# Kernel optimization log

Measured on AMD Instinct MI355X. Metric: run time of the kernel, lower is better.

Reference implementation:

```python
import jax, jax.numpy as jnp
import numpy as np

B, H, S, DK = 4, 16, 4096, 64


def setup_inputs() -> dict:
    key = jax.random.key(0)
    kq, kk, kv = jax.random.split(key, 3)
    Q = jax.random.normal(kq, (B, H, S, DK), dtype=jnp.float32)
    K = jax.random.normal(kk, (B, H, S, DK), dtype=jnp.float32)
    V = jax.random.normal(kv, (B, H, S, DK), dtype=jnp.float32)
    return {"Q": Q, "K": K, "V": V}


def reference(Q, K, V):
    d_k = K.shape[-1]
    inv_sqrt_dk = jnp.sqrt(jnp.float32(1.0) / d_k)
    # [B, H, S, S] materialized scores (faithful to the naive original)
    scores = jnp.einsum('bhqd,bhkd->bhqk', Q, K) * inv_sqrt_dk
    # causal mask: original subtracts (1 - tril) * 1e9 from scores
    s_q, s_k = Q.shape[-2], K.shape[-2]
    causal = jnp.tril(jnp.ones((s_q, s_k), dtype=jnp.float32))
    scores = scores - (1.0 - causal) * 1e9
    probs = jax.nn.softmax(scores, axis=-1)
    out = jnp.einsum('bhqk,bhkd->bhqd', probs, V)
    return out
```

## Files before the change

### kernel.cpp

```cpp
#include <hip/hip_runtime.h>
#include <hip/hip_bf16.h>

typedef short bf16x8 __attribute__((ext_vector_type(8)));
typedef float f32x16 __attribute__((ext_vector_type(16)));
typedef float f32x4v __attribute__((ext_vector_type(4)));

static constexpr int SEQ = 4096;
static constexpr int HD  = 64;
static constexpr int BQ  = 128;
static constexpr int BK  = 64;
static constexpr float QSCALE = 0.125f * 1.44269504088896340736f;

union F8 { bf16x8 v; unsigned short u[8]; uint4 q; };

__device__ __forceinline__ unsigned short f2bf(float x) {
    __bf16 b = (__bf16)x;
    return __builtin_bit_cast(unsigned short, b);
}
__device__ __forceinline__ unsigned pk2(float lo, float hi) {
    return (unsigned)f2bf(lo) | ((unsigned)f2bf(hi) << 16);
}
__device__ __forceinline__ float exp2fast(float x) {
    return __builtin_amdgcn_exp2f(x);
}

__global__ __launch_bounds__(256)
void prep_kv(const float* __restrict__ K, const float* __restrict__ V,
             unsigned short* __restrict__ ws)
{
    __shared__ float vt[64][68];

    const int tid = threadIdx.x;
    const int bid = blockIdx.x;
    const size_t sbase = ((size_t)(bid >> 6)) * (SEQ * HD) +
                         ((size_t)(bid & 63)) * (64 * HD);
    unsigned short* Kt = ws + (size_t)bid * 4096;
    unsigned short* Vt = ws + (size_t)16777216 + (size_t)bid * 4096;

    #pragma unroll
    for (int i = 0; i < 2; ++i) {
        const int c   = tid + 256 * i;
        const int row = c >> 3, j = c & 7;
        const int jsrc = j ^ (row & 7);
        const float* src = K + sbase + row * HD + 8 * jsrc;
        float4 a = *(const float4*)src;
        float4 b = *(const float4*)(src + 4);
        *(uint4*)(Kt + row * 64 + 8 * j) =
            make_uint4(pk2(a.x, a.y), pk2(a.z, a.w), pk2(b.x, b.y), pk2(b.z, b.w));
    }

    {
        const int r  = tid >> 2;
        const int cb = (tid & 3) << 4;
        const float* src = V + sbase + r * HD + cb;
        *(float4*)&vt[r][cb + 0]  = *(const float4*)(src);
        *(float4*)&vt[r][cb + 4]  = *(const float4*)(src + 4);
        *(float4*)&vt[r][cb + 8]  = *(const float4*)(src + 8);
        *(float4*)&vt[r][cb + 12] = *(const float4*)(src + 12);
    }
    __syncthreads();
    #pragma unroll
    for (int i = 0; i < 2; ++i) {
        const int c = tid + 256 * i;
        const int d = c >> 3, j = c & 7;
        const int kb = 8 * (j ^ (d & 7));
        unsigned u[4];
        #pragma unroll
        for (int p = 0; p < 4; ++p)
            u[p] = pk2(vt[kb + 2 * p][d], vt[kb + 2 * p + 1][d]);
        *(uint4*)(Vt + d * 64 + 8 * j) = make_uint4(u[0], u[1], u[2], u[3]);
    }
}

template<bool PRE>
__global__ __launch_bounds__(256, 4)
void mha_fwd(const float* __restrict__ Q, const float* __restrict__ K,
             const float* __restrict__ V, float* __restrict__ O,
             const unsigned short* __restrict__ ws)
{
    __shared__ unsigned short Kl[2][4096];
    __shared__ unsigned short Vl[2][4096];

    const int tid  = threadIdx.x;
    const int lane = tid & 63;
    const int w    = tid >> 6;
    const int l31  = lane & 31;
    const int h    = lane >> 5;

    const int bid = blockIdx.x;
    const int bh  = bid & 63;
    const int qb  = 31 - (bid >> 6);
    const int q0  = qb * BQ;
    const size_t base = (size_t)bh * (SEQ * HD);

    const int qlane  = q0 + 32 * w + l31;
    const int qmax_w = q0 + 32 * w + 31;

    bf16x8 qf[4];
    {
        const float* qrow = Q + base + (size_t)qlane * HD;
        #pragma unroll
        for (int c = 0; c < 4; ++c) {
            const f32x4v x = *(const f32x4v*)(qrow + 16 * c + 8 * h);
            const f32x4v y = *(const f32x4v*)(qrow + 16 * c + 8 * h + 4);
            F8 f;
            #pragma unroll
            for (int j = 0; j < 4; ++j) f.u[j]     = f2bf(x[j] * QSCALE);
            #pragma unroll
            for (int j = 0; j < 4; ++j) f.u[4 + j] = f2bf(y[j] * QSCALE);
            qf[c] = f.v;
        }
    }

    F8 onesf;
    #pragma unroll
    for (int j = 0; j < 8; ++j) onesf.u[j] = 0x3F80;

    f32x16 oacc[2];
    f32x16 lacc;
    #pragma unroll
    for (int r = 0; r < 16; ++r) { oacc[0][r] = 0.f; oacc[1][r] = 0.f; lacc[r] = 0.f; }

    const int nkt = 2 * qb + 2;

    const int ksr = tid >> 2;
    const int ksc = (tid & 3) << 4;
    const int vkb = tid >> 4;
    const int vdb = tid & 15;

    f32x4v kreg[4], vreg[4];

    const unsigned short* Kws = ws;
    const unsigned short* Vws = ws + (size_t)16777216;

    auto stage_pre = [&](int buf, int kt) {
        const size_t toff = (((size_t)bh << 6) + (size_t)kt) << 12;
        #pragma unroll
        for (int i = 0; i < 2; ++i) {
            const int ch = 2 * w + i;
            const unsigned short* kg = Kws + toff + ch * 512 + lane * 8;
            const unsigned short* vg = Vws + toff + ch * 512 + lane * 8;
            __builtin_amdgcn_global_load_lds(
                (const __attribute__((address_space(1))) void*)(const void*)kg,
                (__attribute__((address_space(3))) void*)(void*)&Kl[buf][ch * 512],
                16, 0, 0);
            __builtin_amdgcn_global_load_lds(
                (const __attribute__((address_space(1))) void*)(const void*)vg,
                (__attribute__((address_space(3))) void*)(void*)&Vl[buf][ch * 512],
                16, 0, 0);
        }
    };

    auto load_regs = [&](int kt) {
        const int k0 = kt * BK;
        const float* ks = K + base + (size_t)(k0 + ksr) * HD + ksc;
        kreg[0] = *(const f32x4v*)(ks);
        kreg[1] = *(const f32x4v*)(ks + 4);
        kreg[2] = *(const f32x4v*)(ks + 8);
        kreg[3] = *(const f32x4v*)(ks + 12);
        const float* vs = V + base + (size_t)(k0 + 4 * vkb) * HD + 4 * vdb;
        vreg[0] = *(const f32x4v*)(vs);
        vreg[1] = *(const f32x4v*)(vs + HD);
        vreg[2] = *(const f32x4v*)(vs + 2 * HD);
        vreg[3] = *(const f32x4v*)(vs + 3 * HD);
    };

    auto write_lds = [&](int buf) {
        unsigned u[8];
        #pragma unroll
        for (int i = 0; i < 4; ++i) {
            u[2*i]   = pk2(kreg[i][0], kreg[i][1]);
            u[2*i+1] = pk2(kreg[i][2], kreg[i][3]);
        }
        char* kd = (char*)&Kl[buf][0] + ksr * 128;
        const int o0 = (2 * ksc) ^ ((ksr & 7) << 4);
        *(uint4*)(kd + o0)        = make_uint4(u[0], u[1], u[2], u[3]);
        *(uint4*)(kd + (o0 ^ 16)) = make_uint4(u[4], u[5], u[6], u[7]);
        #pragma unroll
        for (int i = 0; i < 4; ++i) {
            const int c = (i + (vdb >> 1)) & 3;
            const int d = 4 * vdb + c;
            const unsigned lo = pk2(vreg[0][c], vreg[1][c]);
            const unsigned hi = pk2(vreg[2][c], vreg[3][c]);
            char* vd = (char*)&Vl[buf][0] + d * 128 + ((8 * vkb) ^ ((d & 7) << 4));
            *(uint2*)vd = make_uint2(lo, hi);
        }
    };

    if constexpr (PRE) { stage_pre(0, 0); }
    else               { load_regs(0); write_lds(0); }
    __syncthreads();

    for (int kt = 0; kt < nkt; ++kt) {
        const int cur = kt & 1;
        const bool hn = (kt + 1) < nkt;
        if constexpr (PRE) { if (hn) stage_pre(cur ^ 1, kt + 1); }
        else               { if (hn) load_regs(kt + 1); }

        if (64 * kt <= qmax_w) {
            const unsigned short* Kb = &Kl[cur][0];
            const unsigned short* Vb = &Vl[cur][0];
            const int k0 = kt * BK;

            f32x16 sacc[2];
            #pragma unroll
            for (int s = 0; s < 2; ++s)
                #pragma unroll
                for (int r = 0; r < 16; ++r) sacc[s][r] = 0.f;

            #pragma unroll
            for (int s = 0; s < 2; ++s) {
                const int row = 32 * s + l31;
                const char* rp = (const char*)Kb + row * 128;
                const int sw = (row & 7) << 4;
                #pragma unroll
                for (int c = 0; c < 4; ++c) {
                    bf16x8 kf = *(const bf16x8*)(rp + ((32 * c + 16 * h) ^ sw));
                    sacc[s] = __builtin_amdgcn_mfma_f32_32x32x16_bf16(kf, qf[c], sacc[s], 0, 0, 0);
                }
            }

            if (kt >= nkt - 2) {
                #pragma unroll
                for (int s = 0; s < 2; ++s)
                    #pragma unroll
                    for (int r = 0; r < 16; ++r) {
                        const int key = k0 + 32 * s + (r & 3) + 8 * (r >> 2) + 4 * h;
                        if (key > qlane) sacc[s][r] = -1e30f;
                    }
            }

            #pragma unroll
            for (int s = 0; s < 2; ++s)
                #pragma unroll
                for (int r = 0; r < 16; ++r) sacc[s][r] = exp2fast(sacc[s][r]);

            unsigned up[2][8];
            #pragma unroll
            for (int s = 0; s < 2; ++s)
                #pragma unroll
                for (int rr = 0; rr < 8; ++rr)
                    up[s][rr] = pk2(sacc[s][2 * rr], sacc[s][2 * rr + 1]);

            #pragma unroll
            for (int kc = 0; kc < 4; ++kc) {
                const int s  = kc >> 1;
                const int b0 = 4 * (kc & 1);
                const unsigned send0 = h ? up[s][b0]     : up[s][b0 + 2];
                const unsigned send1 = h ? up[s][b0 + 1] : up[s][b0 + 3];
                const unsigned recv0 = __shfl_xor(send0, 32);
                const unsigned recv1 = __shfl_xor(send1, 32);
                F8 pf;
                pf.q.x = h ? recv0         : up[s][b0];
                pf.q.y = h ? recv1         : up[s][b0 + 1];
                pf.q.z = h ? up[s][b0 + 2] : recv0;
                pf.q.w = h ? up[s][b0 + 3] : recv1;
                lacc = __builtin_amdgcn_mfma_f32_32x32x16_bf16(onesf.v, pf.v, lacc, 0, 0, 0);
                #pragma unroll
                for (int dsi = 0; dsi < 2; ++dsi) {
                    const int row = 32 * dsi + l31;
                    const char* vp = (const char*)Vb + row * 128 +
                                     ((32 * kc + 16 * h) ^ ((row & 7) << 4));
                    bf16x8 vf = *(const bf16x8*)vp;
                    oacc[dsi] = __builtin_amdgcn_mfma_f32_32x32x16_bf16(vf, pf.v, oacc[dsi], 0, 0, 0);
                }
            }
        }

        if constexpr (!PRE) { if (hn) write_lds(cur ^ 1); }
        __syncthreads();
    }

    const float il = 1.0f / lacc[0];
    float* orow = O + base + (size_t)qlane * HD;
    #pragma unroll
    for (int dsi = 0; dsi < 2; ++dsi)
        #pragma unroll
        for (int g = 0; g < 4; ++g) {
            f32x4v o4;
            #pragma unroll
            for (int j = 0; j < 4; ++j) o4[j] = oacc[dsi][4 * g + j] * il;
            *(f32x4v*)(orow + 32 * dsi + 8 * g + 4 * h) = o4;
        }
}

extern "C" void kernel_launch(void* const* d_in, const int* in_sizes, int n_in,
                              void* d_out, int out_size, void* d_ws, size_t ws_size,
                              hipStream_t stream) {
    const float* Q = (const float*)d_in[0];
    const float* K = (const float*)d_in[1];
    const float* V = (const float*)d_in[2];
    float* O = (float*)d_out;
    (void)in_sizes; (void)n_in; (void)out_size;

    const size_t need = (size_t)2 * 16777216 * sizeof(unsigned short);
    if (ws_size >= need) {
        unsigned short* ws = (unsigned short*)d_ws;
        prep_kv<<<dim3(64 * 64), 256, 0, stream>>>(K, V, ws);
        mha_fwd<true><<<dim3(32 * 64), 256, 0, stream>>>(Q, K, V, O, ws);
    } else {
        mha_fwd<false><<<dim3(32 * 64), 256, 0, stream>>>(Q, K, V, O, nullptr);
    }
}
```

Measured before the change: 225.6 us.

## Permute K rows so score MFMA output feeds PV MFMA without lane shuffles

K rows are permuted (both in the prep kernel and in the in-kernel LDS write) so the 32x32 score accumulator layout lines up directly with the B-operand layout of the P·V MFMA. This removes the cross-half __shfl_xor exchanges and select logic per kc chunk, and the causal-mask key index formula is updated to match. It also drops the per-tile zeroing of sacc by feeding a constant zero accumulator into the first MFMA, and wraps MFMA groups in s_setprio to favour matrix issue. The risk is mismatched permutation or mask indexing, and priority hints may not help scheduling.

```diff
diff --git a/kernel.cpp b/kernel.cpp
--- a/kernel.cpp
+++ b/kernel.cpp
@@ -22,6 +22,15 @@
 }
 __device__ __forceinline__ float exp2fast(float x) {
     return __builtin_amdgcn_exp2f(x);
+}
+
+__device__ __forceinline__ int kperm_src(int rho) {
+    return (rho & 0x23) | (((rho >> 3) & 1) << 4) |
+           (((rho >> 2) & 1) << 3) | (((rho >> 4) & 1) << 2);
+}
+__device__ __forceinline__ int kperm_dst(int src) {
+    return (src & 0x23) | (((src >> 2) & 1) << 4) |
+           (((src >> 4) & 1) << 3) | (((src >> 3) & 1) << 2);
 }
 
 __global__ __launch_bounds__(256)
@@ -42,7 +51,7 @@
         const int c   = tid + 256 * i;
         const int row = c >> 3, j = c & 7;
         const int jsrc = j ^ (row & 7);
-        const float* src = K + sbase + row * HD + 8 * jsrc;
+        const float* src = K + sbase + kperm_src(row) * HD + 8 * jsrc;
         float4 a = *(const float4*)src;
         float4 b = *(const float4*)(src + 4);
         *(uint4*)(Kt + row * 64 + 8 * j) =
@@ -118,8 +127,11 @@
 
     f32x16 oacc[2];
     f32x16 lacc;
-    #pragma unroll
-    for (int r = 0; r < 16; ++r) { oacc[0][r] = 0.f; oacc[1][r] = 0.f; lacc[r] = 0.f; }
+    f32x16 zacc;
+    #pragma unroll
+    for (int r = 0; r < 16; ++r) {
+        oacc[0][r] = 0.f; oacc[1][r] = 0.f; lacc[r] = 0.f; zacc[r] = 0.f;
+    }
 
     const int nkt = 2 * qb + 2;
 
@@ -172,8 +184,9 @@
             u[2*i]   = pk2(kreg[i][0], kreg[i][1]);
             u[2*i+1] = pk2(kreg[i][2], kreg[i][3]);
         }
-        char* kd = (char*)&Kl[buf][0] + ksr * 128;
-        const int o0 = (2 * ksc) ^ ((ksr & 7) << 4);
+        const int drow = kperm_dst(ksr);
+        char* kd = (char*)&Kl[buf][0] + drow * 128;
+        const int o0 = (2 * ksc) ^ ((drow & 7) << 4);
         *(uint4*)(kd + o0)        = make_uint4(u[0], u[1], u[2], u[3]);
         *(uint4*)(kd + (o0 ^ 16)) = make_uint4(u[4], u[5], u[6], u[7]);
         #pragma unroll
@@ -204,20 +217,18 @@
 
             f32x16 sacc[2];
             #pragma unroll
-            for (int s = 0; s < 2; ++s)
-                #pragma unroll
-                for (int r = 0; r < 16; ++r) sacc[s][r] = 0.f;
-
-            #pragma unroll
             for (int s = 0; s < 2; ++s) {
                 const int row = 32 * s + l31;
                 const char* rp = (const char*)Kb + row * 128;
                 const int sw = (row & 7) << 4;
+                __builtin_amdgcn_s_setprio(1);
                 #pragma unroll
                 for (int c = 0; c < 4; ++c) {
                     bf16x8 kf = *(const bf16x8*)(rp + ((32 * c + 16 * h) ^ sw));
-                    sacc[s] = __builtin_amdgcn_mfma_f32_32x32x16_bf16(kf, qf[c], sacc[s], 0, 0, 0);
+                    sacc[s] = __builtin_amdgcn_mfma_f32_32x32x16_bf16(
+                        kf, qf[c], c == 0 ? zacc : sacc[s], 0, 0, 0);
                 }
+                __builtin_amdgcn_s_setprio(0);
             }
 
             if (kt >= nkt - 2) {
@@ -225,44 +236,36 @@
                 for (int s = 0; s < 2; ++s)
                     #pragma unroll
                     for (int r = 0; r < 16; ++r) {
-                        const int key = k0 + 32 * s + (r & 3) + 8 * (r >> 2) + 4 * h;
+                        const int key = k0 + 32 * s + 16 * ((r >> 2) & 1) +
+                                        4 * ((r >> 3) & 1) + 8 * h + (r & 3);
                         if (key > qlane) sacc[s][r] = -1e30f;
                     }
             }
 
             #pragma unroll
-            for (int s = 0; s < 2; ++s)
+            for (int s = 0; s < 2; ++s) {
                 #pragma unroll
                 for (int r = 0; r < 16; ++r) sacc[s][r] = exp2fast(sacc[s][r]);
 
-            unsigned up[2][8];
-            #pragma unroll
-            for (int s = 0; s < 2; ++s)
                 #pragma unroll
-                for (int rr = 0; rr < 8; ++rr)
-                    up[s][rr] = pk2(sacc[s][2 * rr], sacc[s][2 * rr + 1]);
-
-            #pragma unroll
-            for (int kc = 0; kc < 4; ++kc) {
-                const int s  = kc >> 1;
-                const int b0 = 4 * (kc & 1);
-                const unsigned send0 = h ? up[s][b0]     : up[s][b0 + 2];
-                const unsigned send1 = h ? up[s][b0 + 1] : up[s][b0 + 3];
-                const unsigned recv0 = __shfl_xor(send0, 32);
-                const unsigned recv1 = __shfl_xor(send1, 32);
-                F8 pf;
-                pf.q.x = h ? recv0         : up[s][b0];
-                pf.q.y = h ? recv1         : up[s][b0 + 1];
-                pf.q.z = h ? up[s][b0 + 2] : recv0;
-                pf.q.w = h ? up[s][b0 + 3] : recv1;
-                lacc = __builtin_amdgcn_mfma_f32_32x32x16_bf16(onesf.v, pf.v, lacc, 0, 0, 0);
-                #pragma unroll
-                for (int dsi = 0; dsi < 2; ++dsi) {
-                    const int row = 32 * dsi + l31;
-                    const char* vp = (const char*)Vb + row * 128 +
-                                     ((32 * kc + 16 * h) ^ ((row & 7) << 4));
-                    bf16x8 vf = *(const bf16x8*)vp;
-                    oacc[dsi] = __builtin_amdgcn_mfma_f32_32x32x16_bf16(vf, pf.v, oacc[dsi], 0, 0, 0);
+                for (int m0 = 0; m0 < 2; ++m0) {
+                    const int kc = 2 * s + m0;
+                    F8 pf;
+                    pf.q.x = pk2(sacc[s][4 * m0 + 0],  sacc[s][4 * m0 + 1]);
+                    pf.q.y = pk2(sacc[s][4 * m0 + 2],  sacc[s][4 * m0 + 3]);
+                    pf.q.z = pk2(sacc[s][8 + 4 * m0 + 0], sacc[s][8 + 4 * m0 + 1]);
+                    pf.q.w = pk2(sacc[s][8 + 4 * m0 + 2], sacc[s][8 + 4 * m0 + 3]);
+                    __builtin_amdgcn_s_setprio(1);
+                    lacc = __builtin_amdgcn_mfma_f32_32x32x16_bf16(onesf.v, pf.v, lacc, 0, 0, 0);
+                    #pragma unroll
+                    for (int dsi = 0; dsi < 2; ++dsi) {
+                        const int row = 32 * dsi + l31;
+                        const char* vp = (const char*)Vb + row * 128 +
+                                         ((32 * kc + 16 * h) ^ ((row & 7) << 4));
+                        bf16x8 vf = *(const bf16x8*)vp;
+                        oacc[dsi] = __builtin_amdgcn_mfma_f32_32x32x16_bf16(vf, pf.v, oacc[dsi], 0, 0, 0);
+                    }
+                    __builtin_amdgcn_s_setprio(0);
                 }
             }
         }
```

After: 209.0 us. 1.08x faster.
